# Optimization experiments

Hardware: AMD Instinct MI355X
Metric: run time of the kernel (lower is better)

The kernel has to match this reference:

```python
import jax, jax.numpy as jnp
import numpy as np

NMS_MAX_OUTPUTS = 2000
CLS_SCORE_THRESH = 0.7
IOU_THRESH = 0.3
USE_SIDE_REFINE = False
B, N_ANCHORS, N_VALID, NUM_CLASSES = 4, 20000, 12000, 2


def setup_inputs() -> dict:
    key = jax.random.key(0)
    k = jax.random.split(key, 7)
    deltas = 0.5 * jax.random.normal(k[0], (B, N_ANCHORS, 2), jnp.float32)
    side_deltas = 0.5 * jax.random.normal(k[1], (B, N_ANCHORS, 1), jnp.float32)
    class_logits = 2.0 * jax.random.normal(k[2], (B, N_ANCHORS, NUM_CLASSES), jnp.float32)
    # CTPN-style anchors: fixed width 16, heights in [11, 280], on a ~1600px page
    cx = jax.random.uniform(k[3], (N_VALID,), jnp.float32, 8.0, 1592.0)
    cy = jax.random.uniform(k[4], (N_VALID,), jnp.float32, 0.0, 1600.0)
    h = jax.random.uniform(k[5], (N_VALID,), jnp.float32, 11.0, 280.0)
    valid_anchors = jnp.stack([cx - 8.0, cy - h * 0.5, cx + 8.0, cy + h * 0.5], axis=1)
    valid_indices = jnp.sort(
        jax.random.choice(k[6], N_ANCHORS, (N_VALID,), replace=False)
    ).astype(jnp.int32)
    return {
        "deltas": deltas,
        "side_deltas": side_deltas,
        "class_logits": class_logits,
        "valid_anchors": valid_anchors,
        "valid_indices": valid_indices,
    }


def apply_regress(deltas, side_deltas, anchors, use_side_refine):
    # deltas [B,V,2], side_deltas [B,V,1], anchors [V,4] -> [B,V,4]
    w = anchors[:, 2] - anchors[:, 0]
    h = anchors[:, 3] - anchors[:, 1]
    cx = (anchors[:, 0] + anchors[:, 2]) * 0.5
    cy = (anchors[:, 1] + anchors[:, 3]) * 0.5
    d = jnp.concatenate([deltas, side_deltas], axis=-1) * jnp.array([0.1, 0.2, 0.1], deltas.dtype)
    dy, dh, dx = d[..., 0], d[..., 1], d[..., 2]
    cy = cy + dy * h
    cx = cx + dx * w
    h = h * jnp.exp(dh)
    y1 = cy - h * 0.5
    y2 = cy + h * 0.5
    if use_side_refine:
        x1 = jnp.maximum(cx - w * 0.5, 0.0)
        x2 = cx + w * 0.5
    else:
        x1 = jnp.broadcast_to(anchors[:, 0], y1.shape)
        x2 = jnp.broadcast_to(anchors[:, 2], y1.shape)
    return jnp.stack([x1, y1, x2, y2], axis=-1)


def nms_single(boxes, scores, logits, max_out, iou_t, score_t):
    """Greedy NMS (tf.image.non_max_suppression semantics) + gather + pad_to_fixed_size."""
    V = boxes.shape[0]
    order = jnp.argsort(-jax.lax.stop_gradient(scores))
    b, s, l = boxes[order], scores[order], logits[order]
    bc = jax.lax.stop_gradient(b)  # suppression decisions are non-differentiable
    x1, y1, x2, y2 = bc[:, 0], bc[:, 1], bc[:, 2], bc[:, 3]
    areas = (x2 - x1) * (y2 - y1)
    idxs = jnp.arange(V)
    valid = jax.lax.stop_gradient(s) > score_t

    def body(i, keep):
        xx1 = jnp.maximum(x1[i], x1)
        yy1 = jnp.maximum(y1[i], y1)
        xx2 = jnp.minimum(x2[i], x2)
        yy2 = jnp.minimum(y2[i], y2)
        inter = jnp.maximum(xx2 - xx1, 0.0) * jnp.maximum(yy2 - yy1, 0.0)
        iou = inter / (areas[i] + areas - inter + 1e-10)
        sup = (iou > iou_t) & (idxs > i)
        return jnp.where(keep[i], keep & ~sup, keep)

    keep = jax.lax.fori_loop(0, V, body, valid)
    rank = jnp.cumsum(keep.astype(jnp.int32)) - 1
    sel = keep & (rank < max_out)
    dest = jnp.where(sel, rank, max_out)  # overflow rows parked at row max_out, sliced off
    tag = jnp.ones((V, 1), b.dtype)

    def pad_fixed(x):
        # append tag column of 1s for real rows, scatter to fixed size, zero-pad rest
        aug = jnp.where(sel[:, None], jnp.concatenate([x, tag], axis=1), 0.0)
        out = jnp.zeros((max_out + 1, aug.shape[1]), aug.dtype).at[dest].set(aug)
        return out[:max_out]

    return pad_fixed(b), pad_fixed(s[:, None]), pad_fixed(l)


def reference(deltas, side_deltas, class_logits, valid_anchors, valid_indices):
    d = jnp.take(deltas, valid_indices, axis=1)
    sd = jnp.take(side_deltas, valid_indices, axis=1)
    cl = jnp.take(class_logits, valid_indices, axis=1)
    class_scores = jax.nn.softmax(cl, axis=-1)
    fg_scores = jnp.max(class_scores[..., 1:], axis=-1)  # [B,V]
    proposals = apply_regress(d, sd, valid_anchors, USE_SIDE_REFINE)  # [B,V,4]
    f = lambda bb, ss, ll: nms_single(bb, ss, ll, NMS_MAX_OUTPUTS, IOU_THRESH, CLS_SCORE_THRESH)
    boxes, box_scores, out_logits = jax.vmap(f)(proposals, fg_scores, cl)
    return boxes, box_scores, out_logits
```

## Files before the change

kernel.cpp:

```cpp
#include <hip/hip_runtime.h>
#include <cstdint>
#include <cstddef>

typedef unsigned long long u64;
typedef unsigned int u32;
typedef u32 u32x4 __attribute__((ext_vector_type(4)));

#define AS1 __attribute__((address_space(1)))
#define AS3 __attribute__((address_space(3)))

constexpr int kB = 4;
constexpr int kNA = 20000;
constexpr int kV = 12000;
constexpr int kCAP = 5120;
constexpr int kW = kCAP / 64;
constexpr int kIC = 256;
constexpr int kNCH = kCAP / kIC;
constexpr int kMAXOUT = 2000;
constexpr int kGPB = 20;
constexpr int kMWG = kB * kW * kNCH / 4;
constexpr float kIOU = 0.3f;
constexpr float kSCORE = 0.7f;

static __device__ __forceinline__ u64 greedy64(u64 freeS, u32 d_lo, u32 d_hi) {
  u64 keptS;
  asm volatile(
      "s_mov_b64 s[40:41], %[free]\n\t"
      "s_mov_b64 s[42:43], 0\n\t"
      "GRD_%=:\n\t"
      "s_ff1_i32_b64 s44, s[40:41]\n\t"
      "s_cmp_eq_i32 s44, -1\n\t"
      "s_cbranch_scc1 GRDEND_%=\n\t"
      "s_bitset1_b64 s[42:43], s44\n\t"
      "s_bitset0_b64 s[40:41], s44\n\t"
      "v_readlane_b32 s46, %[dlo], s44\n\t"
      "v_readlane_b32 s47, %[dhi], s44\n\t"
      "s_nop 4\n\t"
      "s_andn2_b64 s[40:41], s[40:41], s[46:47]\n\t"
      "s_branch GRD_%=\n\t"
      "GRDEND_%=:\n\t"
      "s_mov_b64 %[kept], s[42:43]\n\t"
      : [kept] "=&s"(keptS)
      : [free] "s"(freeS), [dlo] "v"(d_lo), [dhi] "v"(d_hi)
      : "s40", "s41", "s42", "s43", "s44", "s45", "s46", "s47", "scc");
  return keptS;
}

__device__ __forceinline__ u64 waveOr64(u64 v) {
  v |= __shfl_xor((unsigned long long)v, 32, 64);
  v |= __shfl_xor((unsigned long long)v, 16, 64);
  v |= __shfl_xor((unsigned long long)v, 8, 64);
  v |= __shfl_xor((unsigned long long)v, 4, 64);
  v |= __shfl_xor((unsigned long long)v, 2, 64);
  v |= __shfl_xor((unsigned long long)v, 1, 64);
  return v;
}

__device__ __forceinline__ u64 readlane64u(u64 v, int l) {
  u32 lo = __builtin_amdgcn_readlane((u32)v, (u32)l);
  u32 hi = __builtin_amdgcn_readlane((u32)(v >> 32), (u32)l);
  return ((u64)hi << 32) | lo;
}

__global__ __launch_bounds__(256) void stage_score(
    const float* __restrict__ deltas, const float* __restrict__ logits,
    const float* __restrict__ anchors, const int* __restrict__ vidx,
    u32* __restrict__ counts, u64* __restrict__ keys,
    float* __restrict__ rec_y1, float* __restrict__ rec_y2,
    float* __restrict__ rec_l0, float* __restrict__ rec_l1) {
  int t = blockIdx.x * 256 + threadIdx.x;
  if (t >= kB * kV) return;
  int b = t / kV, i = t - b * kV;
  int lane = threadIdx.x & 63;
  int idx = vidx[i];
  float2 lg = *(const float2*)(logits + ((size_t)b * kNA + idx) * 2);
  float score = 1.0f / (1.0f + expf(lg.x - lg.y));
  if (!(score > kSCORE)) return;
  float2 dd = *(const float2*)(deltas + ((size_t)b * kNA + idx) * 2);
  float4 a = *(const float4*)(anchors + (size_t)i * 4);
  float h = a.w - a.y;
  float cy = (a.y + a.w) * 0.5f + (dd.x * 0.1f) * h;
  float hn = h * expf(dd.y * 0.2f);
  rec_y1[t] = cy - hn * 0.5f;
  rec_y2[t] = cy + hn * 0.5f;
  rec_l0[t] = lg.x;
  rec_l1[t] = lg.y;
  u64 act = __ballot(1);
  int b0 = (int)__builtin_amdgcn_readfirstlane((u32)b);
  u64 sameb = __ballot(b == b0);
  u64 grp = (b == b0) ? sameb : (act & ~sameb);
  u32 cnt = (u32)__popcll(grp);
  int lead = (int)__ffsll((unsigned long long)grp) - 1;
  u32 base = 0;
  if (lane == lead) base = atomicAdd(&counts[b], cnt);
  base = (u32)__shfl((int)base, lead, 64);
  u32 pos = base + (u32)__popcll(grp & ((1ULL << lane) - 1ULL));
  if (pos < kCAP) {
    u64 key = ((u64)(0xFFFFFFFFu - __float_as_uint(score)) << 32) | (u32)i;
    keys[(size_t)b * kCAP + pos] = key;
  }
}

__global__ __launch_bounds__(256) void rank_sort_emit(
    const u32* __restrict__ counts, const u64* __restrict__ keys,
    const float* __restrict__ rec_y1, const float* __restrict__ rec_y2,
    const float* __restrict__ rec_l0, const float* __restrict__ rec_l1,
    const float* __restrict__ anchors,
    float4* __restrict__ sbox, float* __restrict__ sarea,
    float* __restrict__ ssc, float* __restrict__ sl0, float* __restrict__ sl1) {
  __shared__ u64 sk[kCAP];
  int b = blockIdx.x / (kCAP / 256);
  int chunk = blockIdx.x % (kCAP / 256);
  int tid = threadIdx.x;
  int cnt = (int)min(counts[b], (u32)kCAP);
  for (int e = tid; e < kCAP; e += 256)
    sk[e] = (e < cnt) ? keys[(size_t)b * kCAP + e] : ~0ULL;
  __syncthreads();
  int s = chunk * 256 + tid;
  if (s >= cnt) return;
  u64 ks = sk[s];
  int rank = 0;
  for (int j = 0; j < kCAP; j += 8) {
#pragma unroll
    for (int u = 0; u < 8; ++u) rank += (sk[j + u] < ks) ? 1 : 0;
  }
  int i = (int)(u32)ks;
  float sc = __uint_as_float(0xFFFFFFFFu - (u32)(ks >> 32));
  float x1 = anchors[(size_t)i * 4 + 0], x2 = anchors[(size_t)i * 4 + 2];
  float y1 = rec_y1[b * kV + i], y2 = rec_y2[b * kV + i];
  size_t o = (size_t)b * kCAP + rank;
  sbox[o] = make_float4(x1, y1, x2, y2);
  sarea[o] = (x2 - x1) * (y2 - y1);
  ssc[o] = sc;
  sl0[o] = rec_l0[b * kV + i];
  sl1[o] = rec_l1[b * kV + i];
}

__global__ __launch_bounds__(256) void fused_mask_scan(
    const u32* __restrict__ counts,
    const float4* __restrict__ sbox, const float* __restrict__ sarea,
    u64* __restrict__ mask, u32* __restrict__ colcnt, u64* __restrict__ pub,
    const float* __restrict__ ssc, const float* __restrict__ sl0,
    const float* __restrict__ sl1, float* __restrict__ out) {
  __shared__ float4 sbc[4][kIC];
  __shared__ float sac[4][kIC];
  const int bid = blockIdx.x;

  if (bid < kMWG) {
    int lane = threadIdx.x & 63;
    int wv = threadIdx.x >> 6;
    int gw = bid * 4 + wv;
    int bt = gw & 3;
    int rest = gw >> 2;
    int jb = rest % kW;
    int ic = rest / kW;
    int M = (int)min(counts[bt], (u32)kCAP);
    int W = (M + 63) >> 6;
    if (jb < W) {
      int ibeg = ic * kIC;
      int iend = min(min(M, jb * 64 + 64), ibeg + kIC);
      if (ibeg < iend) {
        const float4* pb = sbox + (size_t)bt * kCAP;
        const float* pa = sarea + (size_t)bt * kCAP;
        u64* mb = mask + (size_t)bt * ((size_t)kW * kCAP);
#pragma unroll
        for (int r = 0; r < kIC / 64; ++r) {
          int e = r * 64 + lane;
          sbc[wv][e] = pb[ibeg + e];
          sac[wv][e] = pa[ibeg + e];
        }
        int j = jb * 64 + lane;
        bool jv = (j < M);
        float4 bj = make_float4(0.f, 0.f, 0.f, 0.f);
        float aj = 0.f;
        if (jv) { bj = pb[j]; aj = pa[j]; }
        for (int b0 = ibeg; b0 < iend; b0 += 64) {
          int lim = min(iend - b0, 64);
          u64 mywm = 0;
#pragma unroll 4
          for (int k = 0; k < lim; ++k) {
            int e = b0 - ibeg + k;
            float4 bi = sbc[wv][e];
            float ai = sac[wv][e];
            float xx1 = fmaxf(bi.x, bj.x);
            float yy1 = fmaxf(bi.y, bj.y);
            float xx2 = fminf(bi.z, bj.z);
            float yy2 = fminf(bi.w, bj.w);
            float inter = fmaxf(xx2 - xx1, 0.0f) * fmaxf(yy2 - yy1, 0.0f);
            float iou = inter / (ai + aj - inter + 1e-10f);
            bool sup = jv && (j > b0 + k) && (iou > kIOU);
            u64 wm = __ballot(sup);
            if (k == lane) mywm = wm;
          }
          if (lane < lim)
            mb[(((size_t)(b0 >> 6)) * kW + jb) * 64 + lane] = mywm;
        }
      }
    }
    if (lane == 0)
      (void)__hip_atomic_fetch_add(&colcnt[bt * kW + jb], 1u, __ATOMIC_RELEASE,
                                   __HIP_MEMORY_SCOPE_AGENT);
    return;
  }

  if (threadIdx.x >= 64) return;
  const int sid = bid - kMWG;
  const int bt = sid & 3;
  const int g = sid >> 2;
  const int lane = threadIdx.x;
  const int M = (int)min(counts[bt], (u32)kCAP);
  const int W = (M + 63) >> 6;
  const int blk0 = 4 * g;
  if (blk0 >= W) return;
  const u64* mb = mask + (size_t)bt * ((size_t)kW * kCAP);
  u64* pp = pub + (size_t)(bt * kGPB) * 8;

#pragma unroll
  for (int c = 0; c < 4; ++c) {
    const u32* cp = &colcnt[bt * kW + 4 * g + c];
    while (__hip_atomic_load(cp, __ATOMIC_ACQUIRE, __HIP_MEMORY_SCOPE_AGENT) <
           (u32)kNCH)
      __builtin_amdgcn_s_sleep(16);
  }

  u64 own[4][4];
#pragma unroll
  for (int J = 0; J < 4; ++J)
#pragma unroll
    for (int q = 0; q < 4; ++q)
      own[J][q] = mb[((size_t)(blk0 + J) * kW + 4 * g + q) * 64 + lane];

  u64 acc0 = 0, acc1 = 0, acc2 = 0, acc3 = 0;
  u32 cum = 0;
  const u64* qa = pp + (size_t)lane * 2;
  const u64* qb = pp + 128 + (size_t)(lane & 15) * 2;
  int next = 0;
  while (next < g) {
    u32x4 ra, rb;
    asm volatile(
        "global_load_dwordx4 %0, %2, off sc0 sc1\n\t"
        "global_load_dwordx4 %1, %3, off sc0 sc1\n\t"
        "s_waitcnt vmcnt(0)"
        : "=&v"(ra), "=&v"(rb)
        : "v"(qa), "v"(qb)
        : "memory");
    u64 wA0 = ((u64)ra[1] << 32) | ra[0];
    u64 wA1 = ((u64)ra[3] << 32) | ra[2];
    u64 wB0 = ((u64)rb[1] << 32) | rb[0];
    u64 wB1 = ((u64)rb[3] << 32) | rb[2];
    u64 okA = __ballot(((wA0 & wA1) >> 63) != 0);
    u64 okB = __ballot(((wB0 & wB1) >> 63) != 0);
    int w = next;
    for (; w < g; ++w) {
      u64 km0, km1, km2, km3;
      if (w < 16) {
        if (((okA >> (4 * w)) & 0xFULL) != 0xFULL) break;
        int L = 4 * w;
        km0 = (u64)(u32)readlane64u(wA0, L)     | ((u64)(u32)readlane64u(wA1, L) << 32);
        km1 = (u64)(u32)readlane64u(wA0, L + 1) | ((u64)(u32)readlane64u(wA1, L + 1) << 32);
        km2 = (u64)(u32)readlane64u(wA0, L + 2) | ((u64)(u32)readlane64u(wA1, L + 2) << 32);
        km3 = (u64)(u32)readlane64u(wA0, L + 3) | ((u64)(u32)readlane64u(wA1, L + 3) << 32);
      } else {
        int L = 4 * (w - 16);
        if (((okB >> L) & 0xFULL) != 0xFULL) break;
        km0 = (u64)(u32)readlane64u(wB0, L)     | ((u64)(u32)readlane64u(wB1, L) << 32);
        km1 = (u64)(u32)readlane64u(wB0, L + 1) | ((u64)(u32)readlane64u(wB1, L + 1) << 32);
        km2 = (u64)(u32)readlane64u(wB0, L + 2) | ((u64)(u32)readlane64u(wB1, L + 2) << 32);
        km3 = (u64)(u32)readlane64u(wB0, L + 3) | ((u64)(u32)readlane64u(wB1, L + 3) << 32);
      }
      cum += (u32)__popcll(km0) + (u32)__popcll(km1) +
             (u32)__popcll(km2) + (u32)__popcll(km3);
      if (km0 | km1 | km2 | km3) {
        u64 v[4][4];
#pragma unroll
        for (int c = 0; c < 4; ++c)
#pragma unroll
          for (int q = 0; q < 4; ++q)
            v[c][q] = mb[((size_t)(4 * w + c) * kW + 4 * g + q) * 64 + lane];
        u64 m0 = -(u64)((km0 >> lane) & 1ULL);
        u64 m1 = -(u64)((km1 >> lane) & 1ULL);
        u64 m2 = -(u64)((km2 >> lane) & 1ULL);
        u64 m3 = -(u64)((km3 >> lane) & 1ULL);
        acc0 |= waveOr64((v[0][0] & m0) | (v[1][0] & m1) | (v[2][0] & m2) | (v[3][0] & m3));
        acc1 |= waveOr64((v[0][1] & m0) | (v[1][1] & m1) | (v[2][1] & m2) | (v[3][1] & m3));
        acc2 |= waveOr64((v[0][2] & m0) | (v[1][2] & m1) | (v[2][2] & m2) | (v[3][2] & m3));
        acc3 |= waveOr64((v[0][3] & m0) | (v[1][3] & m1) | (v[2][3] & m2) | (v[3][3] & m3));
      }
    }
    next = w;
    if (next < g) __builtin_amdgcn_s_sleep(8);
  }

  u64 km[4];
  u32 cums[4];
#define OWN_BLOCK(J, ACC)                                                     \
  {                                                                           \
    const int blk = blk0 + (J);                                               \
    cums[J] = cum;                                                            \
    u64 k = 0;                                                                \
    if (blk < W && (int)cum < kMAXOUT) {                                      \
      int remn = M - blk * 64;                                                \
      u64 validm = (remn >= 64) ? ~0ULL : ((1ULL << remn) - 1ULL);            \
      u64 freeb = ~(ACC)&validm;                                              \
      u32 flo = __builtin_amdgcn_readfirstlane((u32)freeb);                   \
      u32 fhi = __builtin_amdgcn_readfirstlane((u32)(freeb >> 32));           \
      u64 diag = own[J][J];                                                   \
      k = greedy64(((u64)fhi << 32) | flo, (u32)diag, (u32)(diag >> 32));     \
    }                                                                         \
    km[J] = k;                                                                \
    cum += (u32)__popcll(k);                                                  \
  }
  OWN_BLOCK(0, acc0)
  if (km[0]) {
    u64 m = -(u64)((km[0] >> lane) & 1ULL);
    acc1 |= waveOr64(own[0][1] & m);
    acc2 |= waveOr64(own[0][2] & m);
    acc3 |= waveOr64(own[0][3] & m);
  }
  OWN_BLOCK(1, acc1)
  if (km[1]) {
    u64 m = -(u64)((km[1] >> lane) & 1ULL);
    acc2 |= waveOr64(own[1][2] & m);
    acc3 |= waveOr64(own[1][3] & m);
  }
  OWN_BLOCK(2, acc2)
  if (km[2]) {
    u64 m = -(u64)((km[2] >> lane) & 1ULL);
    acc3 |= waveOr64(own[2][3] & m);
  }
  OWN_BLOCK(3, acc3)
#undef OWN_BLOCK

  if (lane == 0) {
    const u64 F = 1ULL << 63;
#pragma unroll
    for (int c = 0; c < 4; ++c) {
      (void)__hip_atomic_fetch_or(&pp[(size_t)g * 8 + 2 * c], F | (u64)(u32)km[c],
                                  __ATOMIC_RELAXED, __HIP_MEMORY_SCOPE_AGENT);
      (void)__hip_atomic_fetch_or(&pp[(size_t)g * 8 + 2 * c + 1],
                                  F | (u64)(u32)(km[c] >> 32),
                                  __ATOMIC_RELAXED, __HIP_MEMORY_SCOPE_AGENT);
    }
  }

  float* boxes = out;
  float* bscores = out + (size_t)kB * kMAXOUT * 5;
  float* blogits = out + (size_t)kB * kMAXOUT * 7;
  auto emit = [&](int i, int rank) {
    size_t o = (size_t)bt * kCAP + i;
    float4 bx = sbox[o];
    size_t t = (size_t)bt * kMAXOUT + rank;
    boxes[t * 5 + 0] = bx.x;
    boxes[t * 5 + 1] = bx.y;
    boxes[t * 5 + 2] = bx.z;
    boxes[t * 5 + 3] = bx.w;
    boxes[t * 5 + 4] = 1.0f;
    bscores[t * 2 + 0] = ssc[o];
    bscores[t * 2 + 1] = 1.0f;
    blogits[t * 3 + 0] = sl0[o];
    blogits[t * 3 + 1] = sl1[o];
    blogits[t * 3 + 2] = 1.0f;
  };
#pragma unroll
  for (int c = 0; c < 4; ++c) {
    if ((km[c] >> lane) & 1ULL) {
      int rank = (int)cums[c] + (int)__popcll(km[c] & ((1ULL << lane) - 1ULL));
      if (rank < kMAXOUT) emit((blk0 + c) * 64 + lane, rank);
    }
  }
}

extern "C" void kernel_launch(void* const* d_in, const int* in_sizes, int n_in,
                              void* d_out, int out_size, void* d_ws, size_t ws_size,
                              hipStream_t stream) {
  const float* deltas = (const float*)d_in[0];
  const float* logits = (const float*)d_in[2];
  const float* anchors = (const float*)d_in[3];
  const int* vidx = (const int*)d_in[4];
  float* out = (float*)d_out;

  char* p = (char*)d_ws;
  auto take = [&](size_t bytes) -> char* {
    char* r = p;
    p += (bytes + 255) & ~(size_t)255;
    return r;
  };
  u32* counts = (u32*)take(kB * sizeof(u32));
  u64* pub = (u64*)take((size_t)kB * kGPB * 8 * sizeof(u64));
  u32* colcnt = (u32*)take((size_t)kB * kW * sizeof(u32));
  u64* keys = (u64*)take((size_t)kB * kCAP * sizeof(u64));
  float* rec_y1 = (float*)take((size_t)kB * kV * sizeof(float));
  float* rec_y2 = (float*)take((size_t)kB * kV * sizeof(float));
  float* rec_l0 = (float*)take((size_t)kB * kV * sizeof(float));
  float* rec_l1 = (float*)take((size_t)kB * kV * sizeof(float));
  float4* sbox = (float4*)take((size_t)kB * kCAP * sizeof(float4));
  float* sarea = (float*)take((size_t)kB * kCAP * sizeof(float));
  float* ssc = (float*)take((size_t)kB * kCAP * sizeof(float));
  float* sl0 = (float*)take((size_t)kB * kCAP * sizeof(float));
  float* sl1 = (float*)take((size_t)kB * kCAP * sizeof(float));
  u64* mask = (u64*)take((size_t)kB * kCAP * kW * sizeof(u64) + 4096);

  (void)hipMemsetAsync(out, 0, (size_t)out_size * sizeof(float), stream);
  (void)hipMemsetAsync(counts, 0, 6656, stream);

  stage_score<<<(kB * kV + 255) / 256, 256, 0, stream>>>(
      deltas, logits, anchors, vidx, counts, keys, rec_y1, rec_y2, rec_l0, rec_l1);
  rank_sort_emit<<<kB * (kCAP / 256), 256, 0, stream>>>(
      counts, keys, rec_y1, rec_y2, rec_l0, rec_l1, anchors,
      sbox, sarea, ssc, sl0, sl1);
  fused_mask_scan<<<kMWG + kB * kGPB, 256, 0, stream>>>(
      counts, sbox, sarea, mask, colcnt, pub, ssc, sl0, sl1, out);
}
```

Baseline: 347.0 us.

## Launch scan blocks first, prefetch mask rows, stage own tiles in LDS

Scan workgroups now take the lowest block IDs so they are resident before the mask-building workgroups, and mask work is reordered column-major so early columns finish first. The chain scan prefetches the next group's 16 mask words while it processes the current one, and the diagonal own tiles are loaded asynchronously into LDS through global_load_lds instead of registers. The goal is to cut the latency of the serial inter-group dependency chain. It risks register pressure from the prefetch buffers and relies on the spinning scan blocks not starving the mask producers.

```diff
diff --git a/kernel.cpp b/kernel.cpp
--- a/kernel.cpp
+++ b/kernel.cpp
@@ -18,6 +18,7 @@
 constexpr int kNCH = kCAP / kIC;
 constexpr int kMAXOUT = 2000;
 constexpr int kGPB = 20;
+constexpr int kSWG = kB * kGPB;
 constexpr int kMWG = kB * kW * kNCH / 4;
 constexpr float kIOU = 0.3f;
 constexpr float kSCORE = 0.7f;
@@ -142,18 +143,19 @@
     u64* __restrict__ mask, u32* __restrict__ colcnt, u64* __restrict__ pub,
     const float* __restrict__ ssc, const float* __restrict__ sl0,
     const float* __restrict__ sl1, float* __restrict__ out) {
-  __shared__ float4 sbc[4][kIC];
-  __shared__ float sac[4][kIC];
+  __shared__ __align__(16) char smem[20480];
   const int bid = blockIdx.x;
 
-  if (bid < kMWG) {
+  if (bid >= kSWG) {
+    float4* sbc = (float4*)smem;
+    float* sac = (float*)(smem + 16384);
     int lane = threadIdx.x & 63;
     int wv = threadIdx.x >> 6;
-    int gw = bid * 4 + wv;
-    int bt = gw & 3;
-    int rest = gw >> 2;
-    int jb = rest % kW;
-    int ic = rest / kW;
+    int gw = (bid - kSWG) * 4 + wv;
+    int jb = gw / (kB * kNCH);
+    int rest = gw - jb * (kB * kNCH);
+    int bt = rest & 3;
+    int ic = rest >> 2;
     int M = (int)min(counts[bt], (u32)kCAP);
     int W = (M + 63) >> 6;
     if (jb < W) {
@@ -166,8 +168,8 @@
 #pragma unroll
         for (int r = 0; r < kIC / 64; ++r) {
           int e = r * 64 + lane;
-          sbc[wv][e] = pb[ibeg + e];
-          sac[wv][e] = pa[ibeg + e];
+          sbc[wv * kIC + e] = pb[ibeg + e];
+          sac[wv * kIC + e] = pa[ibeg + e];
         }
         int j = jb * 64 + lane;
         bool jv = (j < M);
@@ -180,8 +182,8 @@
 #pragma unroll 4
           for (int k = 0; k < lim; ++k) {
             int e = b0 - ibeg + k;
-            float4 bi = sbc[wv][e];
-            float ai = sac[wv][e];
+            float4 bi = sbc[wv * kIC + e];
+            float ai = sac[wv * kIC + e];
             float xx1 = fmaxf(bi.x, bj.x);
             float yy1 = fmaxf(bi.y, bj.y);
             float xx2 = fminf(bi.z, bj.z);
@@ -204,9 +206,9 @@
   }
 
   if (threadIdx.x >= 64) return;
-  const int sid = bid - kMWG;
-  const int bt = sid & 3;
-  const int g = sid >> 2;
+  u64* ownl = (u64*)smem;
+  const int bt = bid & 3;
+  const int g = bid >> 2;
   const int lane = threadIdx.x;
   const int M = (int)min(counts[bt], (u32)kCAP);
   const int W = (M + 63) >> 6;
@@ -223,18 +225,29 @@
       __builtin_amdgcn_s_sleep(16);
   }
 
-  u64 own[4][4];
 #pragma unroll
   for (int J = 0; J < 4; ++J)
 #pragma unroll
-    for (int q = 0; q < 4; ++q)
-      own[J][q] = mb[((size_t)(blk0 + J) * kW + 4 * g + q) * 64 + lane];
+    for (int c = 0; c < 2; ++c)
+      __builtin_amdgcn_global_load_lds(
+          (const AS1 u32*)(mb + ((size_t)(blk0 + J) * kW + 4 * g + 2 * c) * 64 +
+                           (size_t)lane * 2),
+          (AS3 u32*)&ownl[(J * 2 + c) * 128], 16, 0, 0);
 
   u64 acc0 = 0, acc1 = 0, acc2 = 0, acc3 = 0;
   u32 cum = 0;
   const u64* qa = pp + (size_t)lane * 2;
   const u64* qb = pp + 128 + (size_t)(lane & 15) * 2;
+  u64 pv[4][4];
+  auto issuePf = [&](int w) {
+#pragma unroll
+    for (int c = 0; c < 4; ++c)
+#pragma unroll
+      for (int q = 0; q < 4; ++q)
+        pv[c][q] = mb[((size_t)(4 * w + c) * kW + 4 * g + q) * 64 + lane];
+  };
   int next = 0;
+  if (g > 0) issuePf(0);
   while (next < g) {
     u32x4 ra, rb;
     asm volatile(
@@ -250,8 +263,9 @@
     u64 wB1 = ((u64)rb[3] << 32) | rb[2];
     u64 okA = __ballot(((wA0 & wA1) >> 63) != 0);
     u64 okB = __ballot(((wB0 & wB1) >> 63) != 0);
-    int w = next;
-    for (; w < g; ++w) {
+    bool adv = false;
+    while (next < g) {
+      const int w = next;
       u64 km0, km1, km2, km3;
       if (w < 16) {
         if (((okA >> (4 * w)) & 0xFULL) != 0xFULL) break;
@@ -271,28 +285,28 @@
       cum += (u32)__popcll(km0) + (u32)__popcll(km1) +
              (u32)__popcll(km2) + (u32)__popcll(km3);
       if (km0 | km1 | km2 | km3) {
-        u64 v[4][4];
-#pragma unroll
-        for (int c = 0; c < 4; ++c)
-#pragma unroll
-          for (int q = 0; q < 4; ++q)
-            v[c][q] = mb[((size_t)(4 * w + c) * kW + 4 * g + q) * 64 + lane];
         u64 m0 = -(u64)((km0 >> lane) & 1ULL);
         u64 m1 = -(u64)((km1 >> lane) & 1ULL);
         u64 m2 = -(u64)((km2 >> lane) & 1ULL);
         u64 m3 = -(u64)((km3 >> lane) & 1ULL);
-        acc0 |= waveOr64((v[0][0] & m0) | (v[1][0] & m1) | (v[2][0] & m2) | (v[3][0] & m3));
-        acc1 |= waveOr64((v[0][1] & m0) | (v[1][1] & m1) | (v[2][1] & m2) | (v[3][1] & m3));
-        acc2 |= waveOr64((v[0][2] & m0) | (v[1][2] & m1) | (v[2][2] & m2) | (v[3][2] & m3));
-        acc3 |= waveOr64((v[0][3] & m0) | (v[1][3] & m1) | (v[2][3] & m2) | (v[3][3] & m3));
+        acc0 |= waveOr64((pv[0][0] & m0) | (pv[1][0] & m1) | (pv[2][0] & m2) | (pv[3][0] & m3));
+        acc1 |= waveOr64((pv[0][1] & m0) | (pv[1][1] & m1) | (pv[2][1] & m2) | (pv[3][1] & m3));
+        acc2 |= waveOr64((pv[0][2] & m0) | (pv[1][2] & m1) | (pv[2][2] & m2) | (pv[3][2] & m3));
+        acc3 |= waveOr64((pv[0][3] & m0) | (pv[1][3] & m1) | (pv[2][3] & m2) | (pv[3][3] & m3));
       }
+      ++next;
+      if (next < g) issuePf(next);
+      adv = true;
     }
-    next = w;
-    if (next < g) __builtin_amdgcn_s_sleep(8);
-  }
+    if (next < g && !adv) __builtin_amdgcn_s_sleep(8);
+  }
+  __builtin_amdgcn_s_waitcnt(0x0070);
 
   u64 km[4];
   u32 cums[4];
+  auto ownw = [&](int J, int q) -> u64 {
+    return ownl[(J * 2 + (q >> 1)) * 128 + (q & 1) * 64 + lane];
+  };
 #define OWN_BLOCK(J, ACC)                                                     \
   {                                                                           \
     const int blk = blk0 + (J);                                               \
@@ -304,7 +318,7 @@
       u64 freeb = ~(ACC)&validm;                                              \
       u32 flo = __builtin_amdgcn_readfirstlane((u32)freeb);                   \
       u32 fhi = __builtin_amdgcn_readfirstlane((u32)(freeb >> 32));           \
-      u64 diag = own[J][J];                                                   \
+      u64 diag = ownw(J, J);                                                  \
       k = greedy64(((u64)fhi << 32) | flo, (u32)diag, (u32)(diag >> 32));     \
     }                                                                         \
     km[J] = k;                                                                \
@@ -313,20 +327,20 @@
   OWN_BLOCK(0, acc0)
   if (km[0]) {
     u64 m = -(u64)((km[0] >> lane) & 1ULL);
-    acc1 |= waveOr64(own[0][1] & m);
-    acc2 |= waveOr64(own[0][2] & m);
-    acc3 |= waveOr64(own[0][3] & m);
+    acc1 |= waveOr64(ownw(0, 1) & m);
+    acc2 |= waveOr64(ownw(0, 2) & m);
+    acc3 |= waveOr64(ownw(0, 3) & m);
   }
   OWN_BLOCK(1, acc1)
   if (km[1]) {
     u64 m = -(u64)((km[1] >> lane) & 1ULL);
-    acc2 |= waveOr64(own[1][2] & m);
-    acc3 |= waveOr64(own[1][3] & m);
+    acc2 |= waveOr64(ownw(1, 2) & m);
+    acc3 |= waveOr64(ownw(1, 3) & m);
   }
   OWN_BLOCK(2, acc2)
   if (km[2]) {
     u64 m = -(u64)((km[2] >> lane) & 1ULL);
-    acc3 |= waveOr64(own[2][3] & m);
+    acc3 |= waveOr64(ownw(2, 3) & m);
   }
   OWN_BLOCK(3, acc3)
 #undef OWN_BLOCK
@@ -408,6 +422,6 @@
   rank_sort_emit<<<kB * (kCAP / 256), 256, 0, stream>>>(
       counts, keys, rec_y1, rec_y2, rec_l0, rec_l1, anchors,
       sbox, sarea, ssc, sl0, sl1);
-  fused_mask_scan<<<kMWG + kB * kGPB, 256, 0, stream>>>(
+  fused_mask_scan<<<kSWG + kMWG, 256, 0, stream>>>(
       counts, sbox, sarea, mask, colcnt, pub, ssc, sl0, sl1, out);
 }
```

Measured after the change: 346.5 us. About the same (-0.1%).
